# Performance work log

Hardware: AMD Instinct MI355X
Metric: run time of the kernel (lower is better)

The kernel has to match this reference:

```python
import jax, jax.numpy as jnp
import numpy as np

# dims
B, C, N, E = 2048, 3, 32, 256       # batch, views, keypoints, embed_dim
H, L, MLP, P = 8, 3, 1024, 256      # heads, blocks (depth-1), mlp hidden, proj_dim
VIS_KP = 16                          # visible keypoints per sample (constant, as the torch code assumes)
K = VIS_KP + 1                       # + always-visible view token
HD = E // H
SCALE = HD ** -0.5


def _sinusoidal_pe(n, d):
    pos = np.arange(n)[:, None].astype(np.float32)
    i = np.arange(d)[None, :]
    ang = pos / np.power(10000.0, (2 * (i // 2)) / d)
    pe = np.where(i % 2 == 0, np.sin(ang), np.cos(ang))
    return jnp.asarray(pe, dtype=jnp.float32)

PE = _sinusoidal_pe(N, E)  # (N, E)


def layer_norm(x, s, b, eps=1e-5):
    mu = jnp.mean(x, -1, keepdims=True)
    var = jnp.var(x, -1, keepdims=True)
    return (x - mu) * jax.lax.rsqrt(var + eps) * s + b


def _heads(t, T):
    return t.reshape(-1, T, H, HD).transpose(0, 2, 1, 3)  # (S,H,T,HD)


def _gelu(x):
    return jax.nn.gelu(x, approximate=False)


def _mha(x, qkv_w, qkv_b, pw, pb):
    T = x.shape[1]
    q, k, v = jnp.split(x @ qkv_w + qkv_b, 3, axis=-1)
    q, k, v = _heads(q, T), _heads(k, T), _heads(v, T)
    a = jax.nn.softmax(jnp.einsum('shtd,shud->shtu', q, k) * SCALE, -1)
    o = jnp.einsum('shtu,shud->shtd', a, v).transpose(0, 2, 1, 3).reshape(-1, T, E)
    return o @ pw + pb


def reference(x, occlusion_mask, kp_w, kp_b, view_tokens, view_pos,
              ln1_s, ln1_b, qkv_w, qkv_b, ap_w, ap_b, ln2_s, ln2_b,
              fc1_w, fc1_b, fc2_w, fc2_b,
              pool_probe, pool_ln1_s, pool_ln1_b, pool_q_w, pool_q_b,
              pool_kv_w, pool_kv_b, pool_ap_w, pool_ap_b,
              pool_ln2_s, pool_ln2_b, pool_fc1_w, pool_fc1_b,
              pool_fc2_w, pool_fc2_b, pool_out_w, pool_out_b, last_s, last_b):
    # keypoint embedding + sinusoidal positional encoding
    xe = x.reshape(B * C, N, 2) @ kp_w + kp_b + PE[None]
    xe = xe.reshape(B, C, N, E)
    # prepend learnable view tokens (+ view positional embedding)
    vt = jnp.broadcast_to(view_tokens + view_pos, (B, C, 1, E))
    xt = jnp.concatenate([vt, xe], axis=2).reshape(B * C, N + 1, E)
    mask = jnp.concatenate([jnp.ones((B, C, 1, 1), bool), occlusion_mask], axis=2)
    mask = mask.reshape(B * C, N + 1)
    # stream compaction: gather the K visible tokens per sample, order-preserving
    order = jnp.argsort(jnp.where(mask, 0, 1).astype(jnp.int32), axis=1)[:, :K]
    vis = jnp.take_along_axis(xt, order[:, :, None], axis=1)  # (B*C, K, E)
    # pre-norm transformer blocks
    for l in range(L):
        y = vis + _mha(layer_norm(vis, ln1_s[l], ln1_b[l]), qkv_w[l], qkv_b[l], ap_w[l], ap_b[l])
        h = _gelu(layer_norm(y, ln2_s[l], ln2_b[l]) @ fc1_w[l] + fc1_b[l]) @ fc2_w[l] + fc2_b[l]
        vis = y + h
    # attention pooling: learnable probe cross-attends to the sequence
    probe = jnp.broadcast_to(pool_probe, (B * C, 1, E))
    kn = layer_norm(vis, pool_ln1_s, pool_ln1_b)
    q = _heads(probe @ pool_q_w + pool_q_b, 1)
    kk, vv = jnp.split(kn @ pool_kv_w + pool_kv_b, 2, axis=-1)
    kk, vv = _heads(kk, K), _heads(vv, K)
    a = jax.nn.softmax(jnp.einsum('shqd,shkd->shqk', q, kk) * SCALE, -1)
    o = jnp.einsum('shqk,shkd->shqd', a, vv).transpose(0, 2, 1, 3).reshape(B * C, 1, E)
    y = probe + o @ pool_ap_w + pool_ap_b
    y = y + _gelu(layer_norm(y, pool_ln2_s, pool_ln2_b) @ pool_fc1_w + pool_fc1_b) @ pool_fc2_w + pool_fc2_b
    out = (y @ pool_out_w + pool_out_b).reshape(B, C, P)
    return layer_norm(out, last_s, last_b)


def setup_inputs() -> dict:
    key = jax.random.key(0)
    ks = iter(jax.random.split(key, 64))

    def rn(shape, scale=0.02):
        return jax.random.normal(next(ks), shape, jnp.float32) * scale

    x = jax.random.normal(next(ks), (B, C, N, 2), jnp.float32)
    # exactly VIS_KP visible keypoints per sample (torch code assumes constant count)
    rng = np.random.default_rng(0)
    r = rng.random((B, C, N))
    rank = np.argsort(np.argsort(r, axis=-1), axis=-1)
    occlusion_mask = jnp.asarray((rank < VIS_KP)[..., None])
    return dict(
        x=x, occlusion_mask=occlusion_mask,
        kp_w=rn((2, E)), kp_b=jnp.zeros((E,)),
        view_tokens=rn((1, C, 1, E)), view_pos=rn((1, C, 1, E)),
        ln1_s=jnp.ones((L, E)), ln1_b=jnp.zeros((L, E)),
        qkv_w=rn((L, E, 3 * E)), qkv_b=jnp.zeros((L, 3 * E)),
        ap_w=rn((L, E, E)), ap_b=jnp.zeros((L, E)),
        ln2_s=jnp.ones((L, E)), ln2_b=jnp.zeros((L, E)),
        fc1_w=rn((L, E, MLP)), fc1_b=jnp.zeros((L, MLP)),
        fc2_w=rn((L, MLP, E)), fc2_b=jnp.zeros((L, E)),
        pool_probe=rn((1, 1, E)),
        pool_ln1_s=jnp.ones((E,)), pool_ln1_b=jnp.zeros((E,)),
        pool_q_w=rn((E, E)), pool_q_b=jnp.zeros((E,)),
        pool_kv_w=rn((E, 2 * E)), pool_kv_b=jnp.zeros((2 * E,)),
        pool_ap_w=rn((E, E)), pool_ap_b=jnp.zeros((E,)),
        pool_ln2_s=jnp.ones((E,)), pool_ln2_b=jnp.zeros((E,)),
        pool_fc1_w=rn((E, MLP)), pool_fc1_b=jnp.zeros((MLP,)),
        pool_fc2_w=rn((MLP, E)), pool_fc2_b=jnp.zeros((E,)),
        pool_out_w=rn((E, P)), pool_out_b=jnp.zeros((P,)),
        last_s=jnp.ones((P,)), last_b=jnp.zeros((P,)),
    )
```

## Files before the change

kernel.cpp:

```cpp
#include <hip/hip_runtime.h>
#include <hip/hip_bf16.h>
#include <math.h>


#define NB   2048
#define NC   3
#define NN   32
#define NE   256
#define NH   8
#define HDIM 32
#define NL   3
#define NMLP 1024
#define NP   256
#define NK   17
#define NR   (2*NK)
#define NS   (NB*NC)
#define NBLK (NS/2)
#define NT   512
#define NW   8
#define AST  264
#define BHS  520
#define BVS  260

#define T_QKV  6
#define T_PROJ 2
#define T_FC   2
#define T_KV   4

#define SZ_QKV  589824
#define SZ_AP   196608
#define SZ_FC1  786432
#define SZ_FC2  786432
#define SZ_KV   131072
#define OFF_QKV 0
#define OFF_AP  (OFF_QKV + SZ_QKV)
#define OFF_FC1 (OFF_AP + SZ_AP)
#define OFF_FC2 (OFF_FC1 + SZ_FC1)
#define OFF_KV  (OFF_FC2 + SZ_FC2)
#define WTOT    (OFF_KV + SZ_KV)
#define WS_NEEDED ((size_t)WTOT * 2 * 2)

typedef unsigned short u16;
typedef __attribute__((ext_vector_type(8))) short short8;
typedef __attribute__((ext_vector_type(4))) float float4v;

struct Params {
  const void* x; const void* mask;
  const void* kp_w; const void* kp_b;
  const void* view_tokens; const void* view_pos;
  const void* ln1_s; const void* ln1_b;
  const void* qkv_w; const void* qkv_b;
  const void* ap_w; const void* ap_b;
  const void* ln2_s; const void* ln2_b;
  const void* fc1_w; const void* fc1_b;
  const void* fc2_w; const void* fc2_b;
  const void* pool_probe;
  const void* pool_ln1_s; const void* pool_ln1_b;
  const void* pool_q_w; const void* pool_q_b;
  const void* pool_kv_w; const void* pool_kv_b;
  const void* pool_ap_w; const void* pool_ap_b;
// ... 84 lines not shown
                                      u16* __restrict__ Oh, u16* __restrict__ Ol,
                                      const void* __restrict__ gam,
                                      const void* __restrict__ bet) {
  const int lane = threadIdx.x & 63, w = threadIdx.x >> 6;
  for (int t = w; t < NR; t += NW) {
    const float* row = In + t * NE;
    float sum = 0.f, sq = 0.f;
#pragma unroll
    for (int kk = 0; kk < NE / 64; ++kk) {
      const float v = row[lane + 64 * kk];
      sum += v; sq += v * v;
    }
#pragma unroll
    for (int off = 32; off > 0; off >>= 1) {
      sum += __shfl_down(sum, off, 64);
      sq  += __shfl_down(sq,  off, 64);
    }
    sum = __shfl(sum, 0, 64);
    sq  = __shfl(sq,  0, 64);
    const float mu = sum * (1.0f / NE);
    const float r  = rsqrtf(sq * (1.0f / NE) - mu * mu + 1e-5f);
#pragma unroll
    for (int kk = 0; kk < NE / 64; ++kk) {
      const int k = lane + 64 * kk;
      const float v = (row[k] - mu) * r * LD<BF>(gam, k) + LD<BF>(bet, k);
      const u16 hv = cvt16(v);
      Oh[t * AST + k] = hv;
      Ol[t * AST + k] = cvt16(v - b2f(hv));
    }
  }
}

template <bool BF>
__device__ __forceinline__ void mfma4_ws(const u16* __restrict__ Ah,
                                         const u16* __restrict__ Al,
                                         const u16* __restrict__ Wh,
                                         const u16* __restrict__ Wl,
                                         const int kst, const int koff,
                                         const int n0, const int n1,
                                         float4v& D0a, float4v& D1a, float4v& D2a,
                                         float4v& D0b, float4v& D1b, float4v& D2b) {
  const int lane = threadIdx.x & 63;
  const int col = lane & 15, quad = lane >> 4;
  const u16* __restrict__ brh0 = Wh + (size_t)n0 * kst + koff + quad * 8;
  const u16* __restrict__ brl0 = Wl + (size_t)n0 * kst + koff + quad * 8;
  const u16* __restrict__ brh1 = Wh + (size_t)n1 * kst + koff + quad * 8;
  const u16* __restrict__ brl1 = Wl + (size_t)n1 * kst + koff + quad * 8;
  const short8 z8 = {0, 0, 0, 0, 0, 0, 0, 0};
#pragma unroll
  for (int ks = 0; ks < 8; ++ks) {
    const int k0 = ks * 32 + quad * 8;
    const short8 bh0 = *(const short8*)(brh0 + ks * 32);
    const short8 bh1 = *(const short8*)(brh1 + ks * 32);
    short8 bl0, bl1;
    if constexpr (!BF) {
      bl0 = *(const short8*)(brl0 + ks * 32);
      bl1 = *(const short8*)(brl1 + ks * 32);
    }
    const short8 f0h = *(const short8*)(Ah + col * AST + k0);
    const short8 f0l = *(const short8*)(Al + col * AST + k0);
    const short8 f1h = *(const short8*)(Ah + (16 + col) * AST + k0);
    const short8 f1l = *(const short8*)(Al + (16 + col) * AST + k0);
    short8 a2h = z8, a2l = z8;
    if (col < 2) {
      a2h = *(const short8*)(Ah + (32 + col) * AST + k0);
      a2l = *(const short8*)(Al + (32 + col) * AST + k0);
    }
    D0a = __builtin_amdgcn_mfma_f32_16x16x32_bf16(f0h, bh0, D0a, 0, 0, 0);
    D1a = __builtin_amdgcn_mfma_f32_16x16x32_bf16(f1h, bh0, D1a, 0, 0, 0);
    D2a = __builtin_amdgcn_mfma_f32_16x16x32_bf16(a2h, bh0, D2a, 0, 0, 0);
    D0a = __builtin_amdgcn_mfma_f32_16x16x32_bf16(f0l, bh0, D0a, 0, 0, 0);
    D1a = __builtin_amdgcn_mfma_f32_16x16x32_bf16(f1l, bh0, D1a, 0, 0, 0);
    D2a = __builtin_amdgcn_mfma_f32_16x16x32_bf16(a2l, bh0, D2a, 0, 0, 0);
    D0b = __builtin_amdgcn_mfma_f32_16x16x32_bf16(f0h, bh1, D0b, 0, 0, 0);
    D1b = __builtin_amdgcn_mfma_f32_16x16x32_bf16(f1h, bh1, D1b, 0, 0, 0);
    D2b = __builtin_amdgcn_mfma_f32_16x16x32_bf16(a2h, bh1, D2b, 0, 0, 0);
    D0b = __builtin_amdgcn_mfma_f32_16x16x32_bf16(f0l, bh1, D0b, 0, 0, 0);
    D1b = __builtin_amdgcn_mfma_f32_16x16x32_bf16(f1l, bh1, D1b, 0, 0, 0);
    D2b = __builtin_amdgcn_mfma_f32_16x16x32_bf16(a2l, bh1, D2b, 0, 0, 0);
    if constexpr (!BF) {
      D0a = __builtin_amdgcn_mfma_f32_16x16x32_bf16(f0h, bl0, D0a, 0, 0, 0);
      D1a = __builtin_amdgcn_mfma_f32_16x16x32_bf16(f1h, bl0, D1a, 0, 0, 0);
      D2a = __builtin_amdgcn_mfma_f32_16x16x32_bf16(a2h, bl0, D2a, 0, 0, 0);
      D0b = __builtin_amdgcn_mfma_f32_16x16x32_bf16(f0h, bl1, D0b, 0, 0, 0);
      D1b = __builtin_amdgcn_mfma_f32_16x16x32_bf16(f1h, bl1, D1b, 0, 0, 0);
      D2b = __builtin_amdgcn_mfma_f32_16x16x32_bf16(a2h, bl1, D2b, 0, 0, 0);
    }
  }
}

template <bool BF>
__device__ __forceinline__ void mfma2_in(const u16* __restrict__ Ah,
                                         const u16* __restrict__ Al,
                                         const void* __restrict__ W, const int wN,
                                         const int n,
                                         float4v& D0, float4v& D1, float4v& D2) {
  const int lane = threadIdx.x & 63;
  const int col = lane & 15, quad = lane >> 4;
  const short8 z8 = {0, 0, 0, 0, 0, 0, 0, 0};
  for (int ks = 0; ks < 8; ++ks) {
    const int k0 = ks * 32 + quad * 8;
    const short8 f0h = *(const short8*)(Ah + col * AST + k0);
    const short8 f0l = *(const short8*)(Al + col * AST + k0);
    const short8 f1h = *(const short8*)(Ah + (16 + col) * AST + k0);
    const short8 f1l = *(const short8*)(Al + (16 + col) * AST + k0);
    short8 a2h = z8, a2l = z8;
    if (col < 2) {
      a2h = *(const short8*)(Ah + (32 + col) * AST + k0);
      a2l = *(const short8*)(Al + (32 + col) * AST + k0);
    }
    short8 bh, bl;
#pragma unroll
    for (int j2 = 0; j2 < 8; ++j2) {
      const size_t off = (size_t)(k0 + j2) * wN + n;
      if constexpr (BF) {
        bh[j2] = (short)((const u16*)W)[off];
      } else {
        const float wv = ((const float*)W)[off];
        const u16 hv = cvt16(wv);
        bh[j2] = (short)hv;
        bl[j2] = (short)cvt16(wv - b2f(hv));
      }
    }
    D0 = __builtin_amdgcn_mfma_f32_16x16x32_bf16(f0h, bh, D0, 0, 0, 0);
    D1 = __builtin_amdgcn_mfma_f32_16x16x32_bf16(f1h, bh, D1, 0, 0, 0);
    D2 = __builtin_amdgcn_mfma_f32_16x16x32_bf16(a2h, bh, D2, 0, 0, 0);
    D0 = __builtin_amdgcn_mfma_f32_16x16x32_bf16(f0l, bh, D0, 0, 0, 0);
    D1 = __builtin_amdgcn_mfma_f32_16x16x32_bf16(f1l, bh, D1, 0, 0, 0);
    D2 = __builtin_amdgcn_mfma_f32_16x16x32_bf16(a2l, bh, D2, 0, 0, 0);
    if constexpr (!BF) {
      D0 = __builtin_amdgcn_mfma_f32_16x16x32_bf16(f0h, bl, D0, 0, 0, 0);
      D1 = __builtin_amdgcn_mfma_f32_16x16x32_bf16(f1h, bl, D1, 0, 0, 0);
      D2 = __builtin_amdgcn_mfma_f32_16x16x32_bf16(a2h, bl, D2, 0, 0, 0);
    }
  }
}

__device__ __forceinline__ float group_sum(float v, float* sRed, int sid) {
#pragma unroll
  for (int off = 32; off > 0; off >>= 1) v += __shfl_down(v, off, 64);
  __syncthreads();
  if ((threadIdx.x & 63) == 0) sRed[threadIdx.x >> 6] = v;
  __syncthreads();
  return sRed[sid * 4 + 0] + sRed[sid * 4 + 1] +
         sRed[sid * 4 + 2] + sRed[sid * 4 + 3];
}

template <bool BF, bool WS>
__device__ void body(const Params& p, Smem& sm) {
  const int s0  = blockIdx.x * 2;
  const int tid = threadIdx.x;
  const size_t EB = BF ? 2 : 4;
  const int lane = tid & 63, wv_ = tid >> 6, col = lane & 15, quad = lane >> 4;
  const u16* wsh = p.ws;
  const u16* wsl = p.ws + WTOT;
  u16* Hhi = sm.Bh;
  u16* Hlo = (u16*)&sm.Bv[0][0];

  if (tid < 2) {
    const int sid = tid, sg = s0 + sid;
    const unsigned int* mw = (const unsigned int*)p.mask;
    bool byte_layout = false;
    for (int i = 0; i < 8; ++i) {
      const unsigned int w = mw[i];
      if (w != 0u && w != 1u && w != 0x3F800000u) { byte_layout = true; break; }
    }
    int np_ = 0;
// ... 15 lines not shown
    const int th = tid >> 8;
    const float kw0 = LD<BF>(p.kp_w, e);
    const float kw1 = LD<BF>(p.kp_w, NE + e);
    const float kb  = LD<BF>(p.kp_b, e);
    const int   i2  = e & ~1;
    const float freq = expf(-((float)i2 / (float)NE) * logf(10000.0f));
    for (int g = th; g < NR; g += 2) {
      const int sid = (g >= NK) ? 1 : 0;
      const int t   = g - sid * NK;
      const int sg  = s0 + sid;
      const int c   = sg % NC;
      const int n   = sm.Idx[sid][t];
      float v;
      if (n < 0) {
        v = LD<BF>(p.view_tokens, c * NE + e) + LD<BF>(p.view_pos, c * NE + e);
      } else {
        const float x0 = LD<BF>(p.x, (sg * NN + n) * 2 + 0);
        const float x1 = LD<BF>(p.x, (sg * NN + n) * 2 + 1);
        const float ang = (float)n * freq;
        const float pe  = (e & 1) ? cosf(ang) : sinf(ang);
        v = x0 * kw0 + x1 * kw1 + kb + pe;
      }
      sm.X[g][e] = v;
    }
  }
  __syncthreads();

#pragma unroll 1
  for (int l = 0; l < NL; ++l) {
    const void* qkvw = (const char*)p.qkv_w + (size_t)l * NE * 3 * NE * EB;
    const void* qkvb = (const char*)p.qkv_b + (size_t)l * 3 * NE * EB;
    const void* apw  = (const char*)p.ap_w  + (size_t)l * NE * NE * EB;
    const void* apb  = (const char*)p.ap_b  + (size_t)l * NE * EB;
    const void* f1b  = (const char*)p.fc1_b + (size_t)l * NMLP * EB;
    const void* f2bb = (const char*)p.fc2_b + (size_t)l * NE * EB;

    ln_hl<BF>(&sm.X[0][0], sm.Ahi, sm.Alo,
              (const char*)p.ln1_s + (size_t)l * NE * EB,
              (const char*)p.ln1_b + (size_t)l * NE * EB);
    __syncthreads();

    {
      auto wb_qkv = [&](int n, float4v D0, float4v D1, float4v D2) {
        const float bb = LD<BF>(qkvb, n);
#pragma unroll
        for (int r = 0; r < 4; ++r) {
          const int g0 = quad * 4 + r;
          const int g1 = 16 + quad * 4 + r;
          const int g2 = 32 + quad * 4 + r;
          if (n < 512) {
            sm.Bh[g0 * BHS + n] = cvt16(D0[r] + bb);
            sm.Bh[g1 * BHS + n] = cvt16(D1[r] + bb);
            if (g2 < NR) sm.Bh[g2 * BHS + n] = cvt16(D2[r] + bb);
          } else {
            sm.Bv[g0][n - 512] = D0[r] + bb;
            sm.Bv[g1][n - 512] = D1[r] + bb;
            if (g2 < NR) sm.Bv[g2][n - 512] = D2[r] + bb;
          }
        }
      };
#pragma unroll 1
      for (int jj = 0; jj < T_QKV / 2; ++jj) {
        const int n0 = (wv_ + jj * NW) * 16 + col;
        const int n1 = (wv_ + (jj + T_QKV / 2) * NW) * 16 + col;
        float4v D0a = vzero(), D1a = vzero(), D2a = vzero();
        float4v D0b = vzero(), D1b = vzero(), D2b = vzero();
        if constexpr (WS)
          mfma4_ws<BF>(sm.Ahi, sm.Alo,
                       wsh + OFF_QKV + (size_t)l * 196608,
                       wsl + OFF_QKV + (size_t)l * 196608, 256, 0, n0, n1,
                       D0a, D1a, D2a, D0b, D1b, D2b);
        else {
          mfma2_in<BF>(sm.Ahi, sm.Alo, qkvw, 3 * NE, n0, D0a, D1a, D2a);
          mfma2_in<BF>(sm.Ahi, sm.Alo, qkvw, 3 * NE, n1, D0b, D1b, D2b);
        }
        wb_qkv(n0, D0a, D1a, D2a);
        wb_qkv(n1, D0b, D1b, D2b);
      }
    }
    __syncthreads();

    if (tid < 2 * NH * NK) {
      const int sid = tid / (NH * NK);
      const int rem = tid - sid * (NH * NK);
      const int h = rem / NK, t = rem % NK;
      const int gb = sid * NK;
      float q[HDIM];
#pragma unroll
      for (int i8 = 0; i8 < HDIM / 8; ++i8) {
        const short8 qq = *(const short8*)&sm.Bh[(gb + t) * BHS + h * HDIM + i8 * 8];
#pragma unroll
        for (int j = 0; j < 8; ++j) q[i8 * 8 + j] = b2f((u16)qq[j]);
      }
      float sc[NK];
      float mx = -1e30f;
#pragma unroll
      for (int u = 0; u < NK; ++u) {
        float d = 0.f;
#pragma unroll
        for (int i8 = 0; i8 < HDIM / 8; ++i8) {
          const short8 kk = *(const short8*)&sm.Bh[(gb + u) * BHS + 256 + h * HDIM + i8 * 8];
#pragma unroll
          for (int j = 0; j < 8; ++j) d += q[i8 * 8 + j] * b2f((u16)kk[j]);
        }
        d *= 0.17677669529663687f;
        sc[u] = d;
        mx = fmaxf(mx, d);
      }
      float den = 0.f;
#pragma unroll
// ... 11 lines not shown
          o[1] += sc[u] * vv[1];
          o[2] += sc[u] * vv[2];
          o[3] += sc[u] * vv[3];
        }
#pragma unroll
        for (int r = 0; r < 4; ++r) {
          const int jc = h * HDIM + i4 * 4 + r;
          const u16 hv = cvt16(o[r]);
          sm.Ahi[(gb + t) * AST + jc] = hv;
          sm.Alo[(gb + t) * AST + jc] = cvt16(o[r] - b2f(hv));
        }
      }
    }
    __syncthreads();

    {
      auto wb_proj = [&](int n, float4v D0, float4v D1, float4v D2) {
        const float bb = LD<BF>(apb, n);
#pragma unroll
        for (int r = 0; r < 4; ++r) {
          const int g0 = quad * 4 + r;
          const int g1 = 16 + quad * 4 + r;
          const int g2 = 32 + quad * 4 + r;
          sm.X[g0][n] = sm.X[g0][n] + D0[r] + bb;
          sm.X[g1][n] = sm.X[g1][n] + D1[r] + bb;
          if (g2 < NR) sm.X[g2][n] = sm.X[g2][n] + D2[r] + bb;
        }
      };
      const int n0 = wv_ * 16 + col;
      const int n1 = (wv_ + NW) * 16 + col;
      float4v D0a = vzero(), D1a = vzero(), D2a = vzero();
      float4v D0b = vzero(), D1b = vzero(), D2b = vzero();
      if constexpr (WS)
        mfma4_ws<BF>(sm.Ahi, sm.Alo,
                     wsh + OFF_AP + (size_t)l * 65536,
                     wsl + OFF_AP + (size_t)l * 65536, 256, 0, n0, n1,
                     D0a, D1a, D2a, D0b, D1b, D2b);
      else {
        mfma2_in<BF>(sm.Ahi, sm.Alo, apw, NE, n0, D0a, D1a, D2a);
        mfma2_in<BF>(sm.Ahi, sm.Alo, apw, NE, n1, D0b, D1b, D2b);
      }
      wb_proj(n0, D0a, D1a, D2a);
      wb_proj(n1, D0b, D1b, D2b);
    }
    __syncthreads();

    ln_hl<BF>(&sm.X[0][0], sm.Ahi, sm.Alo,
              (const char*)p.ln2_s + (size_t)l * NE * EB,
              (const char*)p.ln2_b + (size_t)l * NE * EB);
    __syncthreads();

#pragma unroll 1
    for (int chunk = 0; chunk < 4; ++chunk) {
      {
        auto wb_fc1 = [&](int n, float4v D0, float4v D1, float4v D2) {
          const float bb = LD<BF>(f1b, chunk * 256 + n);
#pragma unroll
          for (int r = 0; r < 4; ++r) {
            const int g0 = quad * 4 + r;
            const int g1 = 16 + quad * 4 + r;
            const int g2 = 32 + quad * 4 + r;
            {
              const float v = geluf(D0[r] + bb);
              const u16 hv = cvt16(v);
              Hhi[g0 * AST + n] = hv;
              Hlo[g0 * AST + n] = cvt16(v - b2f(hv));
            }
            {
              const float v = geluf(D1[r] + bb);
              const u16 hv = cvt16(v);
              Hhi[g1 * AST + n] = hv;
              Hlo[g1 * AST + n] = cvt16(v - b2f(hv));
            }
            if (g2 < NR) {
              const float v = geluf(D2[r] + bb);
              const u16 hv = cvt16(v);
              Hhi[g2 * AST + n] = hv;
              Hlo[g2 * AST + n] = cvt16(v - b2f(hv));
            }
          }
        };
        const int n0 = wv_ * 16 + col;
        const int n1 = (wv_ + NW) * 16 + col;
        float4v D0a = vzero(), D1a = vzero(), D2a = vzero();
        float4v D0b = vzero(), D1b = vzero(), D2b = vzero();
        if constexpr (WS)
          mfma4_ws<BF>(sm.Ahi, sm.Alo,
                       wsh + OFF_FC1 + (size_t)l * 262144 + (size_t)chunk * 65536,
                       wsl + OFF_FC1 + (size_t)l * 262144 + (size_t)chunk * 65536,
                       256, 0, n0, n1, D0a, D1a, D2a, D0b, D1b, D2b);
        else {
          const void* f1w = (const char*)p.fc1_w +
              ((size_t)l * NE * NMLP + (size_t)chunk * 256) * EB;
          mfma2_in<BF>(sm.Ahi, sm.Alo, f1w, NMLP, n0, D0a, D1a, D2a);
          mfma2_in<BF>(sm.Ahi, sm.Alo, f1w, NMLP, n1, D0b, D1b, D2b);
        }
        wb_fc1(n0, D0a, D1a, D2a);
        wb_fc1(n1, D0b, D1b, D2b);
      }
      __syncthreads();
      {
        auto wb_fc2 = [&](int n, float4v D0, float4v D1, float4v D2) {
          const float bb = (chunk == 0) ? LD<BF>(f2bb, n) : 0.f;
#pragma unroll
          for (int r = 0; r < 4; ++r) {
            const int g0 = quad * 4 + r;
            const int g1 = 16 + quad * 4 + r;
            const int g2 = 32 + quad * 4 + r;
            sm.X[g0][n] = sm.X[g0][n] + D0[r] + bb;
            sm.X[g1][n] = sm.X[g1][n] + D1[r] + bb;
            if (g2 < NR) sm.X[g2][n] = sm.X[g2][n] + D2[r] + bb;
          }
        };
        const int n0 = wv_ * 16 + col;
        const int n1 = (wv_ + NW) * 16 + col;
        float4v D0a = vzero(), D1a = vzero(), D2a = vzero();
        float4v D0b = vzero(), D1b = vzero(), D2b = vzero();
        if constexpr (WS)
          mfma4_ws<BF>(Hhi, Hlo,
                       wsh + OFF_FC2 + (size_t)l * 262144,
                       wsl + OFF_FC2 + (size_t)l * 262144,
                       1024, chunk * 256, n0, n1, D0a, D1a, D2a, D0b, D1b, D2b);
        else {
          const void* f2w = (const char*)p.fc2_w +
              ((size_t)l * NMLP * NE + (size_t)chunk * 256 * NE) * EB;
          mfma2_in<BF>(Hhi, Hlo, f2w, NE, n0, D0a, D1a, D2a);
          mfma2_in<BF>(Hhi, Hlo, f2w, NE, n1, D0b, D1b, D2b);
        }
        wb_fc2(n0, D0a, D1a, D2a);
        wb_fc2(n1, D0b, D1b, D2b);
      }
      __syncthreads();
    }
  }

  ln_hl<BF>(&sm.X[0][0], sm.Ahi, sm.Alo, p.pool_ln1_s, p.pool_ln1_b);
  __syncthreads();
  const int sid = tid >> 8;
  const int j   = tid & (NE - 1);
  {
    float a = LD<BF>(p.pool_q_b, j);
    for (int k = 0; k < NE; k += 4) {
      a += LD<BF>(p.pool_probe, k + 0) * LD<BF>(p.pool_q_w, (k + 0) * NE + j) +
           LD<BF>(p.pool_probe, k + 1) * LD<BF>(p.pool_q_w, (k + 1) * NE + j) +
           LD<BF>(p.pool_probe, k + 2) * LD<BF>(p.pool_q_w, (k + 2) * NE + j) +
           LD<BF>(p.pool_probe, k + 3) * LD<BF>(p.pool_q_w, (k + 3) * NE + j);
    }
    sm.Q[sid][j] = a;
  }
  {
    auto wb_kv = [&](int n, float4v D0, float4v D1, float4v D2) {
      const float bb = LD<BF>(p.pool_kv_b, n);
#pragma unroll
      for (int r = 0; r < 4; ++r) {
        const int g0 = quad * 4 + r;
        const int g1 = 16 + quad * 4 + r;
        const int g2 = 32 + quad * 4 + r;
        if (n < 256) {
          sm.Bh[g0 * BHS + n] = cvt16(D0[r] + bb);
          sm.Bh[g1 * BHS + n] = cvt16(D1[r] + bb);
          if (g2 < NR) sm.Bh[g2 * BHS + n] = cvt16(D2[r] + bb);
        } else {
          sm.Bv[g0][n - 256] = D0[r] + bb;
          sm.Bv[g1][n - 256] = D1[r] + bb;
          if (g2 < NR) sm.Bv[g2][n - 256] = D2[r] + bb;
        }
      }
    };
#pragma unroll 1
    for (int jj = 0; jj < T_KV / 2; ++jj) {
      const int n0 = (wv_ + jj * NW) * 16 + col;
      const int n1 = (wv_ + (jj + T_KV / 2) * NW) * 16 + col;
      float4v D0a = vzero(), D1a = vzero(), D2a = vzero();
      float4v D0b = vzero(), D1b = vzero(), D2b = vzero();
      if constexpr (WS)
        mfma4_ws<BF>(sm.Ahi, sm.Alo, wsh + OFF_KV, wsl + OFF_KV,
                     256, 0, n0, n1, D0a, D1a, D2a, D0b, D1b, D2b);
      else {
        mfma2_in<BF>(sm.Ahi, sm.Alo, p.pool_kv_w, 2 * NE, n0, D0a, D1a, D2a);
        mfma2_in<BF>(sm.Ahi, sm.Alo, p.pool_kv_w, 2 * NE, n1, D0b, D1b, D2b);
      }
      wb_kv(n0, D0a, D1a, D2a);
      wb_kv(n1, D0b, D1b, D2b);
    }
  }
  __syncthreads();
  if (tid < 2 * NH) {
    const int ps = tid >> 3, h = tid & 7;
    const int gb = ps * NK;
    float sc[NK];
    float mx = -1e30f;
#pragma unroll
    for (int u = 0; u < NK; ++u) {
      float d = 0.f;
#pragma unroll
      for (int i8 = 0; i8 < HDIM / 8; ++i8) {
        const short8 kk = *(const short8*)&sm.Bh[(gb + u) * BHS + h * HDIM + i8 * 8];
#pragma unroll
        for (int jx = 0; jx < 8; ++jx)
          d += sm.Q[ps][h * HDIM + i8 * 8 + jx] * b2f((u16)kk[jx]);
      }
      d *= 0.17677669529663687f;
      sc[u] = d;
      mx = fmaxf(mx, d);
    }
    float den = 0.f;
#pragma unroll
    for (int u = 0; u < NK; ++u) { sc[u] = __expf(sc[u] - mx); den += sc[u]; }
    const float inv = 1.0f / den;
#pragma unroll
    for (int u = 0; u < NK; ++u) sm.Pp[ps][h][u] = sc[u] * inv;
  }
  __syncthreads();
  {
    const int h = j >> 5, i = j & 31;
    float o = 0.f;
#pragma unroll
    for (int u = 0; u < NK; ++u)
      o += sm.Pp[sid][h][u] * sm.Bv[sid * NK + u][h * HDIM + i];
    sm.O[sid][j] = o;
  }
  __syncthreads();
  float yv;
  {
    float a = LD<BF>(p.pool_ap_b, j);
    for (int k = 0; k < NE; k += 4) {
      const float4 oo = *(const float4*)&sm.O[sid][k];
      a += oo.x * LD<BF>(p.pool_ap_w, (k + 0) * NE + j) +
           oo.y * LD<BF>(p.pool_ap_w, (k + 1) * NE + j) +
           oo.z * LD<BF>(p.pool_ap_w, (k + 2) * NE + j) +
           oo.w * LD<BF>(p.pool_ap_w, (k + 3) * NE + j);
    }
    yv = LD<BF>(p.pool_probe, j) + a;
  }
  {
    const float s1 = group_sum(yv, sm.Red, sid);
    const float s2 = group_sum(yv * yv, sm.Red, sid);
    const float mu = s1 * (1.0f / NE);
    const float r  = rsqrtf(s2 * (1.0f / NE) - mu * mu + 1e-5f);
    sm.Q[sid][j] = (yv - mu) * r * LD<BF>(p.pool_ln2_s, j) + LD<BF>(p.pool_ln2_b, j);
  }
  __syncthreads();
  float* Hh = (float*)&sm.Bv[0][0];
  {
    float h1[4];
#pragma unroll
    for (int c4 = 0; c4 < 4; ++c4) h1[c4] = LD<BF>(p.pool_fc1_b, c4 * NE + j);
    for (int k = 0; k < NE; k += 4) {
      const float4 nq = *(const float4*)&sm.Q[sid][k];
#pragma unroll
      for (int c4 = 0; c4 < 4; ++c4) {
        const int cjj = c4 * NE + j;
        h1[c4] += nq.x * LD<BF>(p.pool_fc1_w, (k + 0) * NMLP + cjj) +
                  nq.y * LD<BF>(p.pool_fc1_w, (k + 1) * NMLP + cjj) +
                  nq.z * LD<BF>(p.pool_fc1_w, (k + 2) * NMLP + cjj) +
                  nq.w * LD<BF>(p.pool_fc1_w, (k + 3) * NMLP + cjj);
      }
    }
    __syncthreads();
#pragma unroll
    for (int c4 = 0; c4 < 4; ++c4) Hh[sid * NMLP + c4 * NE + j] = geluf(h1[c4]);
  }
  __syncthreads();
  {
    float a = LD<BF>(p.pool_fc2_b, j);
    for (int k = 0; k < NMLP; k += 4) {
      const float4 hh = *(const float4*)&Hh[sid * NMLP + k];
      a += hh.x * LD<BF>(p.pool_fc2_w, (k + 0) * NE + j) +
           hh.y * LD<BF>(p.pool_fc2_w, (k + 1) * NE + j) +
           hh.z * LD<BF>(p.pool_fc2_w, (k + 2) * NE + j) +
           hh.w * LD<BF>(p.pool_fc2_w, (k + 3) * NE + j);
    }
    yv += a;
    sm.RowA[sid][j] = yv;
  }
  __syncthreads();
  float ov;
  {
    float a = LD<BF>(p.pool_out_b, j);
    for (int k = 0; k < NE; k += 4) {
      const float4 yy = *(const float4*)&sm.RowA[sid][k];
      a += yy.x * LD<BF>(p.pool_out_w, (k + 0) * NP + j) +
           yy.y * LD<BF>(p.pool_out_w, (k + 1) * NP + j) +
           yy.z * LD<BF>(p.pool_out_w, (k + 2) * NP + j) +
           yy.w * LD<BF>(p.pool_out_w, (k + 3) * NP + j);
    }
    ov = a;
  }
  {
    const float s1 = group_sum(ov, sm.Red, sid);
    const float s2 = group_sum(ov * ov, sm.Red, sid);
    const float mu = s1 * (1.0f / NP);
    const float r  = rsqrtf(s2 * (1.0f / NP) - mu * mu + 1e-5f);
    const float res = (ov - mu) * r * LD<BF>(p.last_s, j) + LD<BF>(p.last_b, j);
    p.out[(size_t)(s0 + sid) * NP + j] = res;
  }
}

__global__ __launch_bounds__(NT)
__attribute__((amdgpu_waves_per_eu(2, 2)))
void st_encoder_ws(Params p) {
  __shared__ Smem sm;
  const bool isbf = (((const u16*)p.ln1_s)[0] == 0x3F80);
  if (isbf) body<true, true>(p, sm);
  else      body<false, true>(p, sm);
}

__global__ __launch_bounds__(NT)
__attribute__((amdgpu_waves_per_eu(2, 2)))
void st_encoder_nows(Params p) {
  __shared__ Smem sm;
  const bool isbf = (((const u16*)p.ln1_s)[0] == 0x3F80);
// ... 56 lines not shown
```

Measured before the change: 5.253 ms.

## Widen MFMA register tiles to 3-4 column tiles and halve FC chunk count

The QKV GEMM now computes three column tiles per pass over the A fragments, and FC1 and the pool KV projection compute four, so each LDS-loaded activation fragment is reused across more weight tiles. The MLP is processed in two 512-wide chunks instead of four 256-wide ones, with the hidden buffer stride changed to BHS. This cuts LDS fragment reloads and barrier rounds. The costs are more accumulator registers, which may lower occupancy or cause spills, and a larger shared hidden buffer. Unroll pragmas are also added to the scalar pooling-head loops.

```diff
diff --git a/kernel.cpp b/kernel.cpp
--- a/kernel.cpp
+++ b/kernel.cpp
@@ -21,11 +21,6 @@
 #define AST  264
 #define BHS  520
 #define BVS  260
-
-#define T_QKV  6
-#define T_PROJ 2
-#define T_FC   2
-#define T_KV   4
 
 #define SZ_QKV  589824
 #define SZ_AP   196608
@@ -176,87 +171,203 @@
 }
 
 template <bool BF>
-__device__ __forceinline__ void mfma4_ws(const u16* __restrict__ Ah,
+__device__ __forceinline__ void tile9(const short8 f0h, const short8 f0l,
+                                      const short8 f1h, const short8 f1l,
+                                      const short8 a2h, const short8 a2l,
+                                      const short8 bh, const short8 bl,
+                                      float4v& D0, float4v& D1, float4v& D2) {
+  D0 = __builtin_amdgcn_mfma_f32_16x16x32_bf16(f0h, bh, D0, 0, 0, 0);
+  D1 = __builtin_amdgcn_mfma_f32_16x16x32_bf16(f1h, bh, D1, 0, 0, 0);
+  D2 = __builtin_amdgcn_mfma_f32_16x16x32_bf16(a2h, bh, D2, 0, 0, 0);
+  D0 = __builtin_amdgcn_mfma_f32_16x16x32_bf16(f0l, bh, D0, 0, 0, 0);
+  D1 = __builtin_amdgcn_mfma_f32_16x16x32_bf16(f1l, bh, D1, 0, 0, 0);
+  D2 = __builtin_amdgcn_mfma_f32_16x16x32_bf16(a2l, bh, D2, 0, 0, 0);
+  if constexpr (!BF) {
+    D0 = __builtin_amdgcn_mfma_f32_16x16x32_bf16(f0h, bl, D0, 0, 0, 0);
+    D1 = __builtin_amdgcn_mfma_f32_16x16x32_bf16(f1h, bl, D1, 0, 0, 0);
+    D2 = __builtin_amdgcn_mfma_f32_16x16x32_bf16(a2h, bl, D2, 0, 0, 0);
+  }
+}
+
+template <bool BF, int KS, int KST>
+__device__ __forceinline__ void mfmaD_ws(const u16* __restrict__ Ah,
                                          const u16* __restrict__ Al,
+                                         const int ast,
                                          const u16* __restrict__ Wh,
                                          const u16* __restrict__ Wl,
-                                         const int kst, const int koff,
+                                         const int koff,
                                          const int n0, const int n1,
                                          float4v& D0a, float4v& D1a, float4v& D2a,
                                          float4v& D0b, float4v& D1b, float4v& D2b) {
   const int lane = threadIdx.x & 63;
   const int col = lane & 15, quad = lane >> 4;
-  const u16* __restrict__ brh0 = Wh + (size_t)n0 * kst + koff + quad * 8;
-  const u16* __restrict__ brl0 = Wl + (size_t)n0 * kst + koff + quad * 8;
-  const u16* __restrict__ brh1 = Wh + (size_t)n1 * kst + koff + quad * 8;
-  const u16* __restrict__ brl1 = Wl + (size_t)n1 * kst + koff + quad * 8;
+  const u16* __restrict__ b0h = Wh + (size_t)n0 * KST + koff + quad * 8;
+  const u16* __restrict__ b0l = Wl + (size_t)n0 * KST + koff + quad * 8;
+  const u16* __restrict__ b1h = Wh + (size_t)n1 * KST + koff + quad * 8;
+  const u16* __restrict__ b1l = Wl + (size_t)n1 * KST + koff + quad * 8;
   const short8 z8 = {0, 0, 0, 0, 0, 0, 0, 0};
 #pragma unroll
-  for (int ks = 0; ks < 8; ++ks) {
+  for (int ks = 0; ks < KS; ++ks) {
     const int k0 = ks * 32 + quad * 8;
-    const short8 bh0 = *(const short8*)(brh0 + ks * 32);
-    const short8 bh1 = *(const short8*)(brh1 + ks * 32);
-    short8 bl0, bl1;
+    const short8 bh0 = *(const short8*)(b0h + ks * 32);
+    const short8 bh1 = *(const short8*)(b1h + ks * 32);
+    short8 bl0 = z8, bl1 = z8;
     if constexpr (!BF) {
-      bl0 = *(const short8*)(brl0 + ks * 32);
-      bl1 = *(const short8*)(brl1 + ks * 32);
-    }
-    const short8 f0h = *(const short8*)(Ah + col * AST + k0);
-    const short8 f0l = *(const short8*)(Al + col * AST + k0);
-    const short8 f1h = *(const short8*)(Ah + (16 + col) * AST + k0);
-    const short8 f1l = *(const short8*)(Al + (16 + col) * AST + k0);
+      bl0 = *(const short8*)(b0l + ks * 32);
+      bl1 = *(const short8*)(b1l + ks * 32);
+    }
+    const short8 f0h = *(const short8*)(Ah + col * ast + k0);
+    const short8 f0l = *(const short8*)(Al + col * ast + k0);
+    const short8 f1h = *(const short8*)(Ah + (16 + col) * ast + k0);
+    const short8 f1l = *(const short8*)(Al + (16 + col) * ast + k0);
     short8 a2h = z8, a2l = z8;
     if (col < 2) {
-      a2h = *(const short8*)(Ah + (32 + col) * AST + k0);
-      a2l = *(const short8*)(Al + (32 + col) * AST + k0);
-    }
-    D0a = __builtin_amdgcn_mfma_f32_16x16x32_bf16(f0h, bh0, D0a, 0, 0, 0);
-    D1a = __builtin_amdgcn_mfma_f32_16x16x32_bf16(f1h, bh0, D1a, 0, 0, 0);
-    D2a = __builtin_amdgcn_mfma_f32_16x16x32_bf16(a2h, bh0, D2a, 0, 0, 0);
-    D0a = __builtin_amdgcn_mfma_f32_16x16x32_bf16(f0l, bh0, D0a, 0, 0, 0);
-    D1a = __builtin_amdgcn_mfma_f32_16x16x32_bf16(f1l, bh0, D1a, 0, 0, 0);
-    D2a = __builtin_amdgcn_mfma_f32_16x16x32_bf16(a2l, bh0, D2a, 0, 0, 0);
-    D0b = __builtin_amdgcn_mfma_f32_16x16x32_bf16(f0h, bh1, D0b, 0, 0, 0);
-    D1b = __builtin_amdgcn_mfma_f32_16x16x32_bf16(f1h, bh1, D1b, 0, 0, 0);
-    D2b = __builtin_amdgcn_mfma_f32_16x16x32_bf16(a2h, bh1, D2b, 0, 0, 0);
-    D0b = __builtin_amdgcn_mfma_f32_16x16x32_bf16(f0l, bh1, D0b, 0, 0, 0);
-    D1b = __builtin_amdgcn_mfma_f32_16x16x32_bf16(f1l, bh1, D1b, 0, 0, 0);
-    D2b = __builtin_amdgcn_mfma_f32_16x16x32_bf16(a2l, bh1, D2b, 0, 0, 0);
-    if constexpr (!BF) {
-      D0a = __builtin_amdgcn_mfma_f32_16x16x32_bf16(f0h, bl0, D0a, 0, 0, 0);
-      D1a = __builtin_amdgcn_mfma_f32_16x16x32_bf16(f1h, bl0, D1a, 0, 0, 0);
-      D2a = __builtin_amdgcn_mfma_f32_16x16x32_bf16(a2h, bl0, D2a, 0, 0, 0);
-      D0b = __builtin_amdgcn_mfma_f32_16x16x32_bf16(f0h, bl1, D0b, 0, 0, 0);
-      D1b = __builtin_amdgcn_mfma_f32_16x16x32_bf16(f1h, bl1, D1b, 0, 0, 0);
-      D2b = __builtin_amdgcn_mfma_f32_16x16x32_bf16(a2h, bl1, D2b, 0, 0, 0);
-    }
-  }
-}
-
-template <bool BF>
-__device__ __forceinline__ void mfma2_in(const u16* __restrict__ Ah,
+      a2h = *(const short8*)(Ah + (32 + col) * ast + k0);
+      a2l = *(const short8*)(Al + (32 + col) * ast + k0);
+    }
+    tile9<BF>(f0h, f0l, f1h, f1l, a2h, a2l, bh0, bl0, D0a, D1a, D2a);
+    tile9<BF>(f0h, f0l, f1h, f1l, a2h, a2l, bh1, bl1, D0b, D1b, D2b);
+  }
+}
+
+template <bool BF, int KS, int KST>
+__device__ __forceinline__ void mfmaT_ws(const u16* __restrict__ Ah,
                                          const u16* __restrict__ Al,
+                                         const int ast,
+                                         const u16* __restrict__ Wh,
+                                         const u16* __restrict__ Wl,
+                                         const int koff,
+                                         const int n0, const int n1, const int n2,
+                                         float4v& D0a, float4v& D1a, float4v& D2a,
+                                         float4v& D0b, float4v& D1b, float4v& D2b,
+                                         float4v& D0c, float4v& D1c, float4v& D2c) {
+  const int lane = threadIdx.x & 63;
+  const int col = lane & 15, quad = lane >> 4;
+  const u16* __restrict__ b0h = Wh + (size_t)n0 * KST + koff + quad * 8;
+  const u16* __restrict__ b0l = Wl + (size_t)n0 * KST + koff + quad * 8;
+  const u16* __restrict__ b1h = Wh + (size_t)n1 * KST + koff + quad * 8;
+  const u16* __restrict__ b1l = Wl + (size_t)n1 * KST + koff + quad * 8;
+  const u16* __restrict__ b2h = Wh + (size_t)n2 * KST + koff + quad * 8;
+  const u16* __restrict__ b2l = Wl + (size_t)n2 * KST + koff + quad * 8;
+  const short8 z8 = {0, 0, 0, 0, 0, 0, 0, 0};
+#pragma unroll
+  for (int ks = 0; ks < KS; ++ks) {
+    const int k0 = ks * 32 + quad * 8;
+    const short8 f0h = *(const short8*)(Ah + col * ast + k0);
+    const short8 f0l = *(const short8*)(Al + col * ast + k0);
+    const short8 f1h = *(const short8*)(Ah + (16 + col) * ast + k0);
+    const short8 f1l = *(const short8*)(Al + (16 + col) * ast + k0);
+    short8 a2h = z8, a2l = z8;
+    if (col < 2) {
+      a2h = *(const short8*)(Ah + (32 + col) * ast + k0);
+      a2l = *(const short8*)(Al + (32 + col) * ast + k0);
+    }
+    {
+      const short8 bh0 = *(const short8*)(b0h + ks * 32);
+      const short8 bh1 = *(const short8*)(b1h + ks * 32);
+      short8 bl0 = z8, bl1 = z8;
+      if constexpr (!BF) {
+        bl0 = *(const short8*)(b0l + ks * 32);
+        bl1 = *(const short8*)(b1l + ks * 32);
+      }
+      tile9<BF>(f0h, f0l, f1h, f1l, a2h, a2l, bh0, bl0, D0a, D1a, D2a);
+      tile9<BF>(f0h, f0l, f1h, f1l, a2h, a2l, bh1, bl1, D0b, D1b, D2b);
+    }
+    {
+      const short8 bh2 = *(const short8*)(b2h + ks * 32);
+      short8 bl2 = z8;
+      if constexpr (!BF) bl2 = *(const short8*)(b2l + ks * 32);
+      tile9<BF>(f0h, f0l, f1h, f1l, a2h, a2l, bh2, bl2, D0c, D1c, D2c);
+    }
+  }
+}
+
+template <bool BF, int KS, int KST>
+__device__ __forceinline__ void mfmaQ_ws(const u16* __restrict__ Ah,
+                                         const u16* __restrict__ Al,
+                                         const int ast,
+                                         const u16* __restrict__ Wh,
+                                         const u16* __restrict__ Wl,
+                                         const int koff,
+                                         const int n0, const int n1,
+                                         const int n2, const int n3,
+                                         float4v& D0a, float4v& D1a, float4v& D2a,
+                                         float4v& D0b, float4v& D1b, float4v& D2b,
+                                         float4v& D0c, float4v& D1c, float4v& D2c,
+                                         float4v& D0d, float4v& D1d, float4v& D2d) {
+  const int lane = threadIdx.x & 63;
+  const int col = lane & 15, quad = lane >> 4;
+  const u16* __restrict__ b0h = Wh + (size_t)n0 * KST + koff + quad * 8;
+  const u16* __restrict__ b0l = Wl + (size_t)n0 * KST + koff + quad * 8;
+  const u16* __restrict__ b1h = Wh + (size_t)n1 * KST + koff + quad * 8;
+  const u16* __restrict__ b1l = Wl + (size_t)n1 * KST + koff + quad * 8;
+  const u16* __restrict__ b2h = Wh + (size_t)n2 * KST + koff + quad * 8;
+  const u16* __restrict__ b2l = Wl + (size_t)n2 * KST + koff + quad * 8;
+  const u16* __restrict__ b3h = Wh + (size_t)n3 * KST + koff + quad * 8;
+  const u16* __restrict__ b3l = Wl + (size_t)n3 * KST + koff + quad * 8;
+  const short8 z8 = {0, 0, 0, 0, 0, 0, 0, 0};
+#pragma unroll
+  for (int ks = 0; ks < KS; ++ks) {
+    const int k0 = ks * 32 + quad * 8;
+    const short8 f0h = *(const short8*)(Ah + col * ast + k0);
+    const short8 f0l = *(const short8*)(Al + col * ast + k0);
+    const short8 f1h = *(const short8*)(Ah + (16 + col) * ast + k0);
+    const short8 f1l = *(const short8*)(Al + (16 + col) * ast + k0);
+    short8 a2h = z8, a2l = z8;
+    if (col < 2) {
+      a2h = *(const short8*)(Ah + (32 + col) * ast + k0);
+      a2l = *(const short8*)(Al + (32 + col) * ast + k0);
+    }
+    {
+      const short8 bh0 = *(const short8*)(b0h + ks * 32);
+      const short8 bh1 = *(const short8*)(b1h + ks * 32);
+      short8 bl0 = z8, bl1 = z8;
+      if constexpr (!BF) {
+        bl0 = *(const short8*)(b0l + ks * 32);
+        bl1 = *(const short8*)(b1l + ks * 32);
+      }
+      tile9<BF>(f0h, f0l, f1h, f1l, a2h, a2l, bh0, bl0, D0a, D1a, D2a);
+      tile9<BF>(f0h, f0l, f1h, f1l, a2h, a2l, bh1, bl1, D0b, D1b, D2b);
+    }
+    {
+      const short8 bh2 = *(const short8*)(b2h + ks * 32);
+      const short8 bh3 = *(const short8*)(b3h + ks * 32);
+      short8 bl2 = z8, bl3 = z8;
+      if constexpr (!BF) {
+        bl2 = *(const short8*)(b2l + ks * 32);
+        bl3 = *(const short8*)(b3l + ks * 32);
+      }
+      tile9<BF>(f0h, f0l, f1h, f1l, a2h, a2l, bh2, bl2, D0c, D1c, D2c);
+      tile9<BF>(f0h, f0l, f1h, f1l, a2h, a2l, bh3, bl3, D0d, D1d, D2d);
+    }
+  }
+}
+
+template <bool BF, int KS>
+__device__ __forceinline__ void mfma1_in(const u16* __restrict__ Ah,
+                                         const u16* __restrict__ Al,
+                                         const int ast,
                                          const void* __restrict__ W, const int wN,
-                                         const int n,
+                                         const int koff, const int n,
                                          float4v& D0, float4v& D1, float4v& D2) {
   const int lane = threadIdx.x & 63;
   const int col = lane & 15, quad = lane >> 4;
   const short8 z8 = {0, 0, 0, 0, 0, 0, 0, 0};
-  for (int ks = 0; ks < 8; ++ks) {
+  for (int ks = 0; ks < KS; ++ks) {
     const int k0 = ks * 32 + quad * 8;
-    const short8 f0h = *(const short8*)(Ah + col * AST + k0);
-    const short8 f0l = *(const short8*)(Al + col * AST + k0);
-    const short8 f1h = *(const short8*)(Ah + (16 + col) * AST + k0);
-    const short8 f1l = *(const short8*)(Al + (16 + col) * AST + k0);
+    const short8 f0h = *(const short8*)(Ah + col * ast + k0);
+    const short8 f0l = *(const short8*)(Al + col * ast + k0);
+    const short8 f1h = *(const short8*)(Ah + (16 + col) * ast + k0);
+    const short8 f1l = *(const short8*)(Al + (16 + col) * ast + k0);
     short8 a2h = z8, a2l = z8;
     if (col < 2) {
-      a2h = *(const short8*)(Ah + (32 + col) * AST + k0);
-      a2l = *(const short8*)(Al + (32 + col) * AST + k0);
-    }
-    short8 bh, bl;
+      a2h = *(const short8*)(Ah + (32 + col) * ast + k0);
+      a2l = *(const short8*)(Al + (32 + col) * ast + k0);
+    }
+    short8 bh, bl = z8;
 #pragma unroll
     for (int j2 = 0; j2 < 8; ++j2) {
-      const size_t off = (size_t)(k0 + j2) * wN + n;
+      const size_t off = (size_t)(koff + k0 + j2) * wN + n;
       if constexpr (BF) {
         bh[j2] = (short)((const u16*)W)[off];
       } else {
@@ -266,17 +377,7 @@
         bl[j2] = (short)cvt16(wv - b2f(hv));
       }
     }
-    D0 = __builtin_amdgcn_mfma_f32_16x16x32_bf16(f0h, bh, D0, 0, 0, 0);
-    D1 = __builtin_amdgcn_mfma_f32_16x16x32_bf16(f1h, bh, D1, 0, 0, 0);
-    D2 = __builtin_amdgcn_mfma_f32_16x16x32_bf16(a2h, bh, D2, 0, 0, 0);
-    D0 = __builtin_amdgcn_mfma_f32_16x16x32_bf16(f0l, bh, D0, 0, 0, 0);
-    D1 = __builtin_amdgcn_mfma_f32_16x16x32_bf16(f1l, bh, D1, 0, 0, 0);
-    D2 = __builtin_amdgcn_mfma_f32_16x16x32_bf16(a2l, bh, D2, 0, 0, 0);
-    if constexpr (!BF) {
-      D0 = __builtin_amdgcn_mfma_f32_16x16x32_bf16(f0h, bl, D0, 0, 0, 0);
-      D1 = __builtin_amdgcn_mfma_f32_16x16x32_bf16(f1h, bl, D1, 0, 0, 0);
-      D2 = __builtin_amdgcn_mfma_f32_16x16x32_bf16(a2h, bl, D2, 0, 0, 0);
-    }
+    tile9<BF>(f0h, f0l, f1h, f1l, a2h, a2l, bh, bl, D0, D1, D2);
   }
 }
 
@@ -358,7 +459,9 @@
     const void* qkvb = (const char*)p.qkv_b + (size_t)l * 3 * NE * EB;
     const void* apw  = (const char*)p.ap_w  + (size_t)l * NE * NE * EB;
     const void* apb  = (const char*)p.ap_b  + (size_t)l * NE * EB;
+    const void* f1w  = (const char*)p.fc1_w + (size_t)l * NE * NMLP * EB;
     const void* f1b  = (const char*)p.fc1_b + (size_t)l * NMLP * EB;
+    const void* f2w  = (const char*)p.fc2_w + (size_t)l * NMLP * NE * EB;
     const void* f2bb = (const char*)p.fc2_b + (size_t)l * NE * EB;
 
     ln_hl<BF>(&sm.X[0][0], sm.Ahi, sm.Alo,
@@ -386,22 +489,27 @@
         }
       };
 #pragma unroll 1
-      for (int jj = 0; jj < T_QKV / 2; ++jj) {
-        const int n0 = (wv_ + jj * NW) * 16 + col;
-        const int n1 = (wv_ + (jj + T_QKV / 2) * NW) * 16 + col;
+      for (int pass = 0; pass < 2; ++pass) {
+        const int n0 = (wv_ + (pass * 3 + 0) * NW) * 16 + col;
+        const int n1 = (wv_ + (pass * 3 + 1) * NW) * 16 + col;
+        const int n2 = (wv_ + (pass * 3 + 2) * NW) * 16 + col;
         float4v D0a = vzero(), D1a = vzero(), D2a = vzero();
         float4v D0b = vzero(), D1b = vzero(), D2b = vzero();
+        float4v D0c = vzero(), D1c = vzero(), D2c = vzero();
         if constexpr (WS)
-          mfma4_ws<BF>(sm.Ahi, sm.Alo,
-                       wsh + OFF_QKV + (size_t)l * 196608,
-                       wsl + OFF_QKV + (size_t)l * 196608, 256, 0, n0, n1,
-                       D0a, D1a, D2a, D0b, D1b, D2b);
+          mfmaT_ws<BF, 8, 256>(sm.Ahi, sm.Alo, AST,
+                               wsh + OFF_QKV + (size_t)l * 196608,
+                               wsl + OFF_QKV + (size_t)l * 196608, 0,
+                               n0, n1, n2,
+                               D0a, D1a, D2a, D0b, D1b, D2b, D0c, D1c, D2c);
         else {
-          mfma2_in<BF>(sm.Ahi, sm.Alo, qkvw, 3 * NE, n0, D0a, D1a, D2a);
-          mfma2_in<BF>(sm.Ahi, sm.Alo, qkvw, 3 * NE, n1, D0b, D1b, D2b);
+          mfma1_in<BF, 8>(sm.Ahi, sm.Alo, AST, qkvw, 3 * NE, 0, n0, D0a, D1a, D2a);
+          mfma1_in<BF, 8>(sm.Ahi, sm.Alo, AST, qkvw, 3 * NE, 0, n1, D0b, D1b, D2b);
+          mfma1_in<BF, 8>(sm.Ahi, sm.Alo, AST, qkvw, 3 * NE, 0, n2, D0c, D1c, D2c);
         }
         wb_qkv(n0, D0a, D1a, D2a);
         wb_qkv(n1, D0b, D1b, D2b);
+        wb_qkv(n2, D0c, D1c, D2c);
       }
     }
     __syncthreads();
@@ -479,13 +587,13 @@
       float4v D0a = vzero(), D1a = vzero(), D2a = vzero();
       float4v D0b = vzero(), D1b = vzero(), D2b = vzero();
       if constexpr (WS)
-        mfma4_ws<BF>(sm.Ahi, sm.Alo,
-                     wsh + OFF_AP + (size_t)l * 65536,
-                     wsl + OFF_AP + (size_t)l * 65536, 256, 0, n0, n1,
-                     D0a, D1a, D2a, D0b, D1b, D2b);
+        mfmaD_ws<BF, 8, 256>(sm.Ahi, sm.Alo, AST,
+                             wsh + OFF_AP + (size_t)l * 65536,
+                             wsl + OFF_AP + (size_t)l * 65536, 0, n0, n1,
+                             D0a, D1a, D2a, D0b, D1b, D2b);
       else {
-        mfma2_in<BF>(sm.Ahi, sm.Alo, apw, NE, n0, D0a, D1a, D2a);
-        mfma2_in<BF>(sm.Ahi, sm.Alo, apw, NE, n1, D0b, D1b, D2b);
+        mfma1_in<BF, 8>(sm.Ahi, sm.Alo, AST, apw, NE, 0, n0, D0a, D1a, D2a);
+        mfma1_in<BF, 8>(sm.Ahi, sm.Alo, AST, apw, NE, 0, n1, D0b, D1b, D2b);
       }
       wb_proj(n0, D0a, D1a, D2a);
       wb_proj(n1, D0b, D1b, D2b);
@@ -498,10 +606,10 @@
     __syncthreads();
 
 #pragma unroll 1
-    for (int chunk = 0; chunk < 4; ++chunk) {
+    for (int chunk = 0; chunk < 2; ++chunk) {
       {
         auto wb_fc1 = [&](int n, float4v D0, float4v D1, float4v D2) {
-          const float bb = LD<BF>(f1b, chunk * 256 + n);
+          const float bb = LD<BF>(f1b, chunk * 512 + n);
 #pragma unroll
           for (int r = 0; r < 4; ++r) {
             const int g0 = quad * 4 + r;
@@ -510,40 +618,49 @@
             {
               const float v = geluf(D0[r] + bb);
               const u16 hv = cvt16(v);
-              Hhi[g0 * AST + n] = hv;
-              Hlo[g0 * AST + n] = cvt16(v - b2f(hv));
+              Hhi[g0 * BHS + n] = hv;
+              Hlo[g0 * BHS + n] = cvt16(v - b2f(hv));
             }
             {
               const float v = geluf(D1[r] + bb);
               const u16 hv = cvt16(v);
-              Hhi[g1 * AST + n] = hv;
-              Hlo[g1 * AST + n] = cvt16(v - b2f(hv));
+              Hhi[g1 * BHS + n] = hv;
+              Hlo[g1 * BHS + n] = cvt16(v - b2f(hv));
             }
             if (g2 < NR) {
               const float v = geluf(D2[r] + bb);
               const u16 hv = cvt16(v);
-              Hhi[g2 * AST + n] = hv;
-              Hlo[g2 * AST + n] = cvt16(v - b2f(hv));
+              Hhi[g2 * BHS + n] = hv;
+              Hlo[g2 * BHS + n] = cvt16(v - b2f(hv));
             }
           }
         };
-        const int n0 = wv_ * 16 + col;
-        const int n1 = (wv_ + NW) * 16 + col;
+        const int n0 = (wv_ + 0 * NW) * 16 + col;
+        const int n1 = (wv_ + 1 * NW) * 16 + col;
+        const int n2 = (wv_ + 2 * NW) * 16 + col;
+        const int n3 = (wv_ + 3 * NW) * 16 + col;
         float4v D0a = vzero(), D1a = vzero(), D2a = vzero();
         float4v D0b = vzero(), D1b = vzero(), D2b = vzero();
+        float4v D0c = vzero(), D1c = vzero(), D2c = vzero();
+        float4v D0d = vzero(), D1d = vzero(), D2d = vzero();
         if constexpr (WS)
-          mfma4_ws<BF>(sm.Ahi, sm.Alo,
-                       wsh + OFF_FC1 + (size_t)l * 262144 + (size_t)chunk * 65536,
-                       wsl + OFF_FC1 + (size_t)l * 262144 + (size_t)chunk * 65536,
-                       256, 0, n0, n1, D0a, D1a, D2a, D0b, D1b, D2b);
+          mfmaQ_ws<BF, 8, 256>(sm.Ahi, sm.Alo, AST,
+                               wsh + OFF_FC1 + (size_t)l * 262144 + (size_t)chunk * 131072,
+                               wsl + OFF_FC1 + (size_t)l * 262144 + (size_t)chunk * 131072,
+                               0, n0, n1, n2, n3,
+                               D0a, D1a, D2a, D0b, D1b, D2b,
+                               D0c, D1c, D2c, D0d, D1d, D2d);
         else {
-          const void* f1w = (const char*)p.fc1_w +
-              ((size_t)l * NE * NMLP + (size_t)chunk * 256) * EB;
-          mfma2_in<BF>(sm.Ahi, sm.Alo, f1w, NMLP, n0, D0a, D1a, D2a);
-          mfma2_in<BF>(sm.Ahi, sm.Alo, f1w, NMLP, n1, D0b, D1b, D2b);
+          const void* f1wc = (const char*)f1w + (size_t)chunk * 512 * EB;
+          mfma1_in<BF, 8>(sm.Ahi, sm.Alo, AST, f1wc, NMLP, 0, n0, D0a, D1a, D2a);
+          mfma1_in<BF, 8>(sm.Ahi, sm.Alo, AST, f1wc, NMLP, 0, n1, D0b, D1b, D2b);
+          mfma1_in<BF, 8>(sm.Ahi, sm.Alo, AST, f1wc, NMLP, 0, n2, D0c, D1c, D2c);
+          mfma1_in<BF, 8>(sm.Ahi, sm.Alo, AST, f1wc, NMLP, 0, n3, D0d, D1d, D2d);
         }
         wb_fc1(n0, D0a, D1a, D2a);
         wb_fc1(n1, D0b, D1b, D2b);
+        wb_fc1(n2, D0c, D1c, D2c);
+        wb_fc1(n3, D0d, D1d, D2d);
       }
       __syncthreads();
       {
@@ -564,15 +681,14 @@
         float4v D0a = vzero(), D1a = vzero(), D2a = vzero();
         float4v D0b = vzero(), D1b = vzero(), D2b = vzero();
         if constexpr (WS)
-          mfma4_ws<BF>(Hhi, Hlo,
-                       wsh + OFF_FC2 + (size_t)l * 262144,
-                       wsl + OFF_FC2 + (size_t)l * 262144,
-                       1024, chunk * 256, n0, n1, D0a, D1a, D2a, D0b, D1b, D2b);
+          mfmaD_ws<BF, 16, 1024>(Hhi, Hlo, BHS,
+                                 wsh + OFF_FC2 + (size_t)l * 262144,
+                                 wsl + OFF_FC2 + (size_t)l * 262144,
+                                 chunk * 512, n0, n1,
+                                 D0a, D1a, D2a, D0b, D1b, D2b);
         else {
-          const void* f2w = (const char*)p.fc2_w +
-              ((size_t)l * NMLP * NE + (size_t)chunk * 256 * NE) * EB;
-          mfma2_in<BF>(Hhi, Hlo, f2w, NE, n0, D0a, D1a, D2a);
-          mfma2_in<BF>(Hhi, Hlo, f2w, NE, n1, D0b, D1b, D2b);
+          mfma1_in<BF, 16>(Hhi, Hlo, BHS, f2w, NE, chunk * 512, n0, D0a, D1a, D2a);
+          mfma1_in<BF, 16>(Hhi, Hlo, BHS, f2w, NE, chunk * 512, n1, D0b, D1b, D2b);
         }
         wb_fc2(n0, D0a, D1a, D2a);
         wb_fc2(n1, D0b, D1b, D2b);
@@ -587,6 +703,7 @@
   const int j   = tid & (NE - 1);
   {
     float a = LD<BF>(p.pool_q_b, j);
+#pragma unroll 4
     for (int k = 0; k < NE; k += 4) {
       a += LD<BF>(p.pool_probe, k + 0) * LD<BF>(p.pool_q_w, (k + 0) * NE + j) +
            LD<BF>(p.pool_probe, k + 1) * LD<BF>(p.pool_q_w, (k + 1) * NE + j) +
@@ -614,22 +731,29 @@
         }
       }
     };
-#pragma unroll 1
-    for (int jj = 0; jj < T_KV / 2; ++jj) {
-      const int n0 = (wv_ + jj * NW) * 16 + col;
-      const int n1 = (wv_ + (jj + T_KV / 2) * NW) * 16 + col;
-      float4v D0a = vzero(), D1a = vzero(), D2a = vzero();
-      float4v D0b = vzero(), D1b = vzero(), D2b = vzero();
-      if constexpr (WS)
-        mfma4_ws<BF>(sm.Ahi, sm.Alo, wsh + OFF_KV, wsl + OFF_KV,
-                     256, 0, n0, n1, D0a, D1a, D2a, D0b, D1b, D2b);
-      else {
-        mfma2_in<BF>(sm.Ahi, sm.Alo, p.pool_kv_w, 2 * NE, n0, D0a, D1a, D2a);
-        mfma2_in<BF>(sm.Ahi, sm.Alo, p.pool_kv_w, 2 * NE, n1, D0b, D1b, D2b);
-      }
-      wb_kv(n0, D0a, D1a, D2a);
-      wb_kv(n1, D0b, D1b, D2b);
-    }
+    const int n0 = (wv_ + 0 * NW) * 16 + col;
+    const int n1 = (wv_ + 1 * NW) * 16 + col;
+    const int n2 = (wv_ + 2 * NW) * 16 + col;
+    const int n3 = (wv_ + 3 * NW) * 16 + col;
+    float4v D0a = vzero(), D1a = vzero(), D2a = vzero();
+    float4v D0b = vzero(), D1b = vzero(), D2b = vzero();
+    float4v D0c = vzero(), D1c = vzero(), D2c = vzero();
+    float4v D0d = vzero(), D1d = vzero(), D2d = vzero();
+    if constexpr (WS)
+      mfmaQ_ws<BF, 8, 256>(sm.Ahi, sm.Alo, AST, wsh + OFF_KV, wsl + OFF_KV,
+                           0, n0, n1, n2, n3,
+                           D0a, D1a, D2a, D0b, D1b, D2b,
+                           D0c, D1c, D2c, D0d, D1d, D2d);
+    else {
+      mfma1_in<BF, 8>(sm.Ahi, sm.Alo, AST, p.pool_kv_w, 2 * NE, 0, n0, D0a, D1a, D2a);
+      mfma1_in<BF, 8>(sm.Ahi, sm.Alo, AST, p.pool_kv_w, 2 * NE, 0, n1, D0b, D1b, D2b);
+      mfma1_in<BF, 8>(sm.Ahi, sm.Alo, AST, p.pool_kv_w, 2 * NE, 0, n2, D0c, D1c, D2c);
+      mfma1_in<BF, 8>(sm.Ahi, sm.Alo, AST, p.pool_kv_w, 2 * NE, 0, n3, D0d, D1d, D2d);
+    }
+    wb_kv(n0, D0a, D1a, D2a);
+    wb_kv(n1, D0b, D1b, D2b);
+    wb_kv(n2, D0c, D1c, D2c);
+    wb_kv(n3, D0d, D1d, D2d);
   }
   __syncthreads();
   if (tid < 2 * NH) {
@@ -671,6 +795,7 @@
   float yv;
   {
     float a = LD<BF>(p.pool_ap_b, j);
+#pragma unroll 4
     for (int k = 0; k < NE; k += 4) {
       const float4 oo = *(const float4*)&sm.O[sid][k];
       a += oo.x * LD<BF>(p.pool_ap_w, (k + 0) * NE + j) +
@@ -693,6 +818,7 @@
     float h1[4];
 #pragma unroll
     for (int c4 = 0; c4 < 4; ++c4) h1[c4] = LD<BF>(p.pool_fc1_b, c4 * NE + j);
+#pragma unroll 4
     for (int k = 0; k < NE; k += 4) {
       const float4 nq = *(const float4*)&sm.Q[sid][k];
 #pragma unroll
@@ -711,6 +837,7 @@
   __syncthreads();
   {
     float a = LD<BF>(p.pool_fc2_b, j);
+#pragma unroll 4
     for (int k = 0; k < NMLP; k += 4) {
       const float4 hh = *(const float4*)&Hh[sid * NMLP + k];
       a += hh.x * LD<BF>(p.pool_fc2_w, (k + 0) * NE + j) +
@@ -725,6 +852,7 @@
   float ov;
   {
     float a = LD<BF>(p.pool_out_b, j);
+#pragma unroll 4
     for (int k = 0; k < NE; k += 4) {
       const float4 yy = *(const float4*)&sm.RowA[sid][k];
       a += yy.x * LD<BF>(p.pool_out_w, (k + 0) * NP + j) +
```

Measured after the change: 5.505 ms. +4.8%, slower.
